# Kernel optimization log

Hardware: AMD Instinct MI355X
Metric: run time of the kernel (lower is better)

Reference implementation:

```python
import jax, jax.numpy as jnp
import numpy as np

VOXEL_DIM = (64, 64, 64)
VOXEL_SIZE = 0.04
STRIDE = 4.0  # backbone2d_stride


def setup_inputs() -> dict:
    key = jax.random.key(0)
    k1, k2 = jax.random.split(key, 2)
    bs, nv, cin, h, w = 4, 12, 384, 64, 64
    cout = 32
    vit_feats = jax.random.normal(k1, (bs, nv, cin, h, w), dtype=jnp.float32)
    w_reduce = jax.random.normal(k2, (cout, cin), dtype=jnp.float32) * 0.05
    b_reduce = jnp.zeros((cout,), dtype=jnp.float32)
    # Realistic pinhole projections: K @ [I | t], camera ~3m from grid center.
    rng = np.random.default_rng(0)
    f, cx, cy = 128.0, 128.0, 128.0
    K = np.array([[f, 0.0, cx], [0.0, f, cy], [0.0, 0.0, 1.0]])
    projs = np.zeros((bs, nv, 3, 4), dtype=np.float32)
    for v in range(nv):
        t = np.array([0.2 * rng.standard_normal(), 0.2 * rng.standard_normal(),
                      3.0 + 0.3 * rng.standard_normal()])
        E = np.concatenate([np.eye(3), t[:, None]], axis=1)  # 3x4
        projs[:, v] = (K @ E).astype(np.float32)
    return {"vit_feats": vit_feats, "w_reduce": w_reduce,
            "b_reduce": b_reduce, "projection": jnp.asarray(projs)}


def _backproject(proj, feats):
    """proj: (b,3,4), feats: (b,c,h,w) -> volume (b,c,N), valid (b,N)."""
    nx, ny, nz = VOXEL_DIM
    N = nx * ny * nz
    b, c, h, w = feats.shape
    X, Y, Z = jnp.meshgrid(jnp.arange(nx), jnp.arange(ny), jnp.arange(nz), indexing='ij')
    coords = jnp.stack([X.ravel(), Y.ravel(), Z.ravel()]).astype(feats.dtype)  # (3, N)
    origin = jnp.array([[-nx * VOXEL_SIZE / 2],
                        [-ny * VOXEL_SIZE / 2],
                        [-nz * VOXEL_SIZE / 2]], dtype=feats.dtype)
    world = coords * VOXEL_SIZE + origin                    # (3, N)
    world = jnp.concatenate([world, jnp.ones((1, N), feats.dtype)], axis=0)  # (4, N)
    cam = jnp.einsum('bij,jn->bin', proj, world)            # (b, 3, N)
    px = jnp.round(cam[:, 0] / cam[:, 2]).astype(jnp.int32)
    py = jnp.round(cam[:, 1] / cam[:, 2]).astype(jnp.int32)
    pz = cam[:, 2]
    valid = (px >= 0) & (py >= 0) & (px < w) & (py < h) & (pz > 0)  # (b, N)
    pxc = jnp.clip(px, 0, w - 1)
    pyc = jnp.clip(py, 0, h - 1)
    # per-batch gather: feats[b, :, py, px]
    gath = jax.vmap(lambda f, yy, xx: f[:, yy, xx])(feats, pyc, pxc)  # (b, c, N)
    vol = jnp.where(valid[:, None, :], gath, jnp.zeros((), feats.dtype))
    return vol, valid


def reference(vit_feats, w_reduce, b_reduce, projection):
    bs, nv, cin, h, w = vit_feats.shape
    cout = w_reduce.shape[0]
    nx, ny, nz = VOXEL_DIM
    N = nx * ny * nz
    # 1x1 conv channel reduction
    feats = jnp.einsum('bnchw,oc->bnohw', vit_feats, w_reduce) \
            + b_reduce[None, None, :, None, None]
    # divide intrinsics rows by the 2D backbone stride
    proj = projection.at[:, :, :2, :].set(projection[:, :, :2, :] / STRIDE)
    feats_v = jnp.moveaxis(feats, 1, 0)   # (nv, b, c, h, w)
    proj_v = jnp.moveaxis(proj, 1, 0)     # (nv, b, 3, 4)

    def step(carry, xs):
        vol, cnt = carry
        p, f = xs
        v, m = _backproject(p, f)
        return (vol + v, cnt + m.astype(vol.dtype)), None

    vol0 = jnp.zeros((bs, cout, N), jnp.float32)
    cnt0 = jnp.zeros((bs, N), jnp.float32)
    (vol, cnt), _ = jax.lax.scan(step, (vol0, cnt0), (proj_v, feats_v))
    # volume / valid, zeroed where never observed
    cnt_b = cnt[:, None, :]
    out = jnp.where(cnt_b > 0, vol / jnp.maximum(cnt_b, 1.0), jnp.zeros((), vol.dtype))
    return out.reshape(bs, cout, nx, ny, nz)
```

## Files before the change

### kernel.cpp

```cpp
#include <hip/hip_runtime.h>

#define NV 12
#define CIN 384
#define COUT 32
#define HW 4096
#define NVOX 262144
#define KSTEPS 12
#define KSTEP 32
#define PIXB 128
#define ZROW_U4 786432

typedef __attribute__((ext_vector_type(8))) short short8v;
typedef __attribute__((ext_vector_type(4))) short short4v;
typedef __attribute__((ext_vector_type(4))) float f32x4;

__device__ __forceinline__ short bf16b(float x) {
    union { float f; unsigned u; } c; c.f = x;
    unsigned r = (c.u + 0x7fffu + ((c.u >> 16) & 1u)) >> 16;
    return (short)r;
}

__device__ __forceinline__ void load_lds16(const float* g, float* l) {
    __builtin_amdgcn_global_load_lds(
        (const __attribute__((address_space(1))) void*)g,
        (__attribute__((address_space(3))) void*)l, 16, 0, 0);
}

__global__ __launch_bounds__(256) void w_prep_kernel(
    const float* __restrict__ w, short* __restrict__ wfrag,
    short* __restrict__ feats)
{
    const int t = blockIdx.x * 256 + threadIdx.x;
    if (t < 48 * 32) {
        const int sg = t >> 5, o = t & 31;
        const int s = sg >> 2, g = sg & 3;
        short8v v;
#pragma unroll
        for (int i = 0; i < 8; ++i)
            v[i] = bf16b(w[o * CIN + s * 32 + g * 8 + i]);
        *reinterpret_cast<short8v*>(wfrag + t * 8) = v;
    } else if (t >= 1536 && t < 1540) {
        reinterpret_cast<uint4*>(feats)[ZROW_U4 + (t - 1536)] =
            make_uint4(0u, 0u, 0u, 0u);
    }
}

__global__ __launch_bounds__(256) void mv_reduce_mfma_kernel(
    const float* __restrict__ vit, const short* __restrict__ wfrag,
    const float* __restrict__ bias, short* __restrict__ feats)
{
    __shared__ float lds[KSTEP][PIXB];

    const int bid  = blockIdx.x;
    const int bv   = bid >> 5;
    const int pix0 = (bid & 31) * PIXB;

    const int tid  = threadIdx.x;
    const int wave = tid >> 6;
    const int l    = tid & 63;
    const int col  = l & 15;
    const int g    = l >> 4;
    const int lhalf = l >> 5;
    const int lq    = l & 31;
    const int srcq  = (lq - 2 * wave) & 31;

    const float* vbase = vit + (size_t)bv * CIN * HW + pix0;
    const short8v* wf  = reinterpret_cast<const short8v*>(wfrag);

    const int rc0 = (wave * 32 + col + 8 * g) & 127;
    const int rc1 = (wave * 32 + col + 16 + 8 * g) & 127;

    f32x4 acc00 = {0.f, 0.f, 0.f, 0.f};
    f32x4 acc01 = {0.f, 0.f, 0.f, 0.f};
    f32x4 acc10 = {0.f, 0.f, 0.f, 0.f};
    f32x4 acc11 = {0.f, 0.f, 0.f, 0.f};

#pragma unroll
    for (int i = 0; i < 4; ++i) {
        const int row = 8 * wave + 2 * i;
        load_lds16(vbase + (size_t)(row + lhalf) * HW + srcq * 4, &lds[row][0]);
    }

#pragma unroll
    for (int s = 0; s < KSTEPS; ++s) {
        __syncthreads();

        float fr0[8], fr1[8];
#pragma unroll
        for (int i = 0; i < 8; ++i) {
            fr0[i] = lds[8 * g + i][rc0];
            fr1[i] = lds[8 * g + i][rc1];
        }
        __syncthreads();

        if (s + 1 < KSTEPS) {
#pragma unroll
            for (int i = 0; i < 4; ++i) {
                const int row = 8 * wave + 2 * i;
                load_lds16(vbase + (size_t)((s + 1) * KSTEP + row + lhalf) * HW
                               + srcq * 4,
                           &lds[row][0]);
            }
        }

        short8v bfr0, bfr1;
#pragma unroll
        for (int i = 0; i < 8; ++i) {
            bfr0[i] = bf16b(fr0[i]);
            bfr1[i] = bf16b(fr1[i]);
        }

        const short8v a0 = wf[(s * 4 + g) * 32 + col];
        const short8v a1 = wf[(s * 4 + g) * 32 + 16 + col];

        acc00 = __builtin_amdgcn_mfma_f32_16x16x32_bf16(a0, bfr0, acc00, 0, 0, 0);
        acc01 = __builtin_amdgcn_mfma_f32_16x16x32_bf16(a1, bfr0, acc01, 0, 0, 0);
        acc10 = __builtin_amdgcn_mfma_f32_16x16x32_bf16(a0, bfr1, acc10, 0, 0, 0);
        acc11 = __builtin_amdgcn_mfma_f32_16x16x32_bf16(a1, bfr1, acc11, 0, 0, 0);
    }

    const float4 b0 = *reinterpret_cast<const float4*>(bias + 4 * g);
    const float4 b1 = *reinterpret_cast<const float4*>(bias + 16 + 4 * g);
    short* dst0 = feats + ((size_t)bv * HW + pix0 + wave * 32 + col) * COUT;
    short* dst1 = dst0 + 16 * COUT;
    short4v o00, o01, o10, o11;
    o00[0] = bf16b(acc00[0] + b0.x); o00[1] = bf16b(acc00[1] + b0.y);
    o00[2] = bf16b(acc00[2] + b0.z); o00[3] = bf16b(acc00[3] + b0.w);
    o01[0] = bf16b(acc01[0] + b1.x); o01[1] = bf16b(acc01[1] + b1.y);
    o01[2] = bf16b(acc01[2] + b1.z); o01[3] = bf16b(acc01[3] + b1.w);
    o10[0] = bf16b(acc10[0] + b0.x); o10[1] = bf16b(acc10[1] + b0.y);
    o10[2] = bf16b(acc10[2] + b0.z); o10[3] = bf16b(acc10[3] + b0.w);
    o11[0] = bf16b(acc11[0] + b1.x); o11[1] = bf16b(acc11[1] + b1.y);
    o11[2] = bf16b(acc11[2] + b1.z); o11[3] = bf16b(acc11[3] + b1.w);
    *reinterpret_cast<short4v*>(dst0 + 4 * g) = o00;
    *reinterpret_cast<short4v*>(dst0 + 16 + 4 * g) = o01;
    *reinterpret_cast<short4v*>(dst1 + 4 * g) = o10;
    *reinterpret_cast<short4v*>(dst1 + 16 + 4 * g) = o11;
}

__global__ __launch_bounds__(256) void mv_fuse_kernel(
    const unsigned short* __restrict__ feats, const float* __restrict__ proj,
    float* __restrict__ out)
{
    __shared__ double P[NV][12];

    const int tid = threadIdx.x;
    const unsigned gid = blockIdx.x * 256u + tid;
    const unsigned vox = gid >> 2;
    const int r = tid & 3;
    const int lane = tid & 63;
    const int b = vox >> 18;
    const int n = vox & (NVOX - 1);

    if (tid < NV * 12) {
        const int v = tid / 12, e = tid - v * 12;
        const int row = e >> 2;
        const float s = (row < 2) ? 0.25f : 1.0f;
        P[v][e] = (double)(proj[((b * NV + v) * 3 + row) * 4 + (e & 3)] * s);
    }
    __syncthreads();

    const int k = n & 63, j = (n >> 6) & 63, i = n >> 12;
    const double wx = (double)i * 0.04 - 1.28;
    const double wy = (double)j * 0.04 - 1.28;
    const double wz = (double)k * 0.04 - 1.28;

    int off[3];
    int cnt = 0;
    const int bbase = b * (NV * HW * 4);
#pragma unroll
    for (int s = 0; s < 3; ++s) {
        const double* p = P[4 * s + r];
        const double cz = p[8] * wx + p[9] * wy + p[10] * wz + p[11];
        const double cx = p[0] * wx + p[1] * wy + p[2] * wz + p[3];
        const double cy = p[4] * wx + p[5] * wy + p[6] * wz + p[7];
        const double rcz = 1.0 / cz;
        const double u = rint(cx * rcz);
        const double t = rint(cy * rcz);
        const bool valid = (cz > 0.0) & (u >= 0.0) & (u <= 63.0) &
                           (t >= 0.0) & (t <= 63.0);
        const double uc = fmin(fmax(u, 0.0), 63.0);
        const double tc = fmin(fmax(t, 0.0), 63.0);
        const int pix = (int)uc + 64 * (int)tc;
        off[s] = valid ? (bbase + ((4 * s + r) * HW + pix) * 4) : ZROW_U4;
        cnt += valid ? 1 : 0;
    }
    cnt += __shfl_xor(cnt, 1);
    cnt += __shfl_xor(cnt, 2);

    float acc[8];
#pragma unroll
    for (int q = 0; q < 8; ++q) acc[q] = 0.0f;

    const uint4* f4 = reinterpret_cast<const uint4*>(feats);
#pragma unroll
    for (int v = 0; v < NV; ++v) {
        const int src = (lane & ~3) | (v & 3);
        const int ov = __shfl(off[v >> 2], src, 64);
        const uint4 u4 = f4[ov + r];
        acc[0] += __uint_as_float(u4.x << 16);
        acc[1] += __uint_as_float(u4.x & 0xffff0000u);
        acc[2] += __uint_as_float(u4.y << 16);
        acc[3] += __uint_as_float(u4.y & 0xffff0000u);
        acc[4] += __uint_as_float(u4.z << 16);
        acc[5] += __uint_as_float(u4.z & 0xffff0000u);
        acc[6] += __uint_as_float(u4.w << 16);
        acc[7] += __uint_as_float(u4.w & 0xffff0000u);
    }

    const float sc = (cnt > 0) ? (1.0f / (float)cnt) : 0.0f;
    float* ob = out + (size_t)b * COUT * NVOX + (size_t)(8 * r) * NVOX + n;
#pragma unroll
    for (int q = 0; q < 8; ++q)
        ob[(size_t)q * NVOX] = acc[q] * sc;
}

extern "C" void kernel_launch(void* const* d_in, const int* in_sizes, int n_in,
                              void* d_out, int out_size, void* d_ws, size_t ws_size,
                              hipStream_t stream) {
    const float* vit  = (const float*)d_in[0];
    const float* w    = (const float*)d_in[1];
    const float* bias = (const float*)d_in[2];
    const float* proj = (const float*)d_in[3];
    float* out = (float*)d_out;

    short* wfrag = (short*)d_ws;
    short* feats = (short*)((char*)d_ws + 48 * 32 * 8 * 2);

    w_prep_kernel<<<7, 256, 0, stream>>>(w, wfrag, feats);

    mv_reduce_mfma_kernel<<<1536, 256, 0, stream>>>(vit, wfrag, bias, feats);

    mv_fuse_kernel<<<16384, 256, 0, stream>>>(
        (const unsigned short*)feats, proj, out);
}
```

Baseline: 125.6 us.

## Double-buffer LDS staging with explicit vmcnt waits in reduce kernel

Result: no change. 125.8 us (+0.2%).

```diff
diff --git a/kernel.cpp b/kernel.cpp
--- a/kernel.cpp
+++ b/kernel.cpp
@@ -45,11 +45,11 @@
     }
 }
 
-__global__ __launch_bounds__(256) void mv_reduce_mfma_kernel(
+__global__ __launch_bounds__(256, 5) void mv_reduce_mfma_kernel(
     const float* __restrict__ vit, const short* __restrict__ wfrag,
     const float* __restrict__ bias, short* __restrict__ feats)
 {
-    __shared__ float lds[KSTEP][PIXB];
+    __shared__ float lds[2][KSTEP][PIXB];
 
     const int bid  = blockIdx.x;
     const int bv   = bid >> 5;
@@ -75,33 +75,43 @@
     f32x4 acc10 = {0.f, 0.f, 0.f, 0.f};
     f32x4 acc11 = {0.f, 0.f, 0.f, 0.f};
 
-#pragma unroll
-    for (int i = 0; i < 4; ++i) {
-        const int row = 8 * wave + 2 * i;
-        load_lds16(vbase + (size_t)(row + lhalf) * HW + srcq * 4, &lds[row][0]);
-    }
+#define STAGE(s, b)                                                        \
+    {                                                                      \
+        _Pragma("unroll")                                                  \
+        for (int i_ = 0; i_ < 4; ++i_) {                                   \
+            const int row_ = 8 * wave + 2 * i_;                            \
+            load_lds16(vbase + (size_t)((s) * KSTEP + row_ + lhalf) * HW   \
+                           + srcq * 4,                                     \
+                       &lds[b][row_][0]);                                  \
+        }                                                                  \
+    }
+
+    STAGE(0, 0)
+    STAGE(1, 1)
+    short8v a0c = wf[(0 * 4 + g) * 32 + col];
+    short8v a1c = wf[(0 * 4 + g) * 32 + 16 + col];
 
 #pragma unroll
     for (int s = 0; s < KSTEPS; ++s) {
-        __syncthreads();
+        if (s == KSTEPS - 1) asm volatile("s_waitcnt vmcnt(2)" ::: "memory");
+        else                 asm volatile("s_waitcnt vmcnt(6)" ::: "memory");
+        __builtin_amdgcn_s_barrier();
 
         float fr0[8], fr1[8];
 #pragma unroll
         for (int i = 0; i < 8; ++i) {
-            fr0[i] = lds[8 * g + i][rc0];
-            fr1[i] = lds[8 * g + i][rc1];
+            fr0[i] = lds[s & 1][8 * g + i][rc0];
+            fr1[i] = lds[s & 1][8 * g + i][rc1];
         }
-        __syncthreads();
-
+        asm volatile("s_waitcnt lgkmcnt(0)" ::: "memory");
+        __builtin_amdgcn_s_barrier();
+
+        short8v a0n = a0c, a1n = a1c;
         if (s + 1 < KSTEPS) {
-#pragma unroll
-            for (int i = 0; i < 4; ++i) {
-                const int row = 8 * wave + 2 * i;
-                load_lds16(vbase + (size_t)((s + 1) * KSTEP + row + lhalf) * HW
-                               + srcq * 4,
-                           &lds[row][0]);
-            }
+            a0n = wf[((s + 1) * 4 + g) * 32 + col];
+            a1n = wf[((s + 1) * 4 + g) * 32 + 16 + col];
         }
+        if (s + 2 < KSTEPS) STAGE(s + 2, s & 1)
 
         short8v bfr0, bfr1;
 #pragma unroll
@@ -110,14 +120,14 @@
             bfr1[i] = bf16b(fr1[i]);
         }
 
-        const short8v a0 = wf[(s * 4 + g) * 32 + col];
-        const short8v a1 = wf[(s * 4 + g) * 32 + 16 + col];
-
-        acc00 = __builtin_amdgcn_mfma_f32_16x16x32_bf16(a0, bfr0, acc00, 0, 0, 0);
-        acc01 = __builtin_amdgcn_mfma_f32_16x16x32_bf16(a1, bfr0, acc01, 0, 0, 0);
-        acc10 = __builtin_amdgcn_mfma_f32_16x16x32_bf16(a0, bfr1, acc10, 0, 0, 0);
-        acc11 = __builtin_amdgcn_mfma_f32_16x16x32_bf16(a1, bfr1, acc11, 0, 0, 0);
-    }
+        acc00 = __builtin_amdgcn_mfma_f32_16x16x32_bf16(a0c, bfr0, acc00, 0, 0, 0);
+        acc01 = __builtin_amdgcn_mfma_f32_16x16x32_bf16(a1c, bfr0, acc01, 0, 0, 0);
+        acc10 = __builtin_amdgcn_mfma_f32_16x16x32_bf16(a0c, bfr1, acc10, 0, 0, 0);
+        acc11 = __builtin_amdgcn_mfma_f32_16x16x32_bf16(a1c, bfr1, acc11, 0, 0, 0);
+
+        a0c = a0n; a1c = a1n;
+    }
+#undef STAGE
 
     const float4 b0 = *reinterpret_cast<const float4*>(bias + 4 * g);
     const float4 b1 = *reinterpret_cast<const float4*>(bias + 16 + 4 * g);
```
